# Kernel tuning notes

Hardware: AMD Instinct MI355X
Metric: run time of the kernel (lower is better)

Reference implementation:

```python
import jax, jax.numpy as jnp
import numpy as np

B, W, C, H = 2, 2048, 1024, 16
K = C // H  # 64
LN_EPS = 1e-5


def setup_inputs() -> dict:
    key = jax.random.key(0)
    ks = jax.random.split(key, 8)
    return {
        "seq1": jax.random.normal(ks[0], (B, W, C), jnp.float32),
        "seq2": jax.random.normal(ks[1], (B, W, C), jnp.float32),
        "ln_gamma": jnp.ones((C,), jnp.float32),
        "ln_beta": jnp.zeros((C,), jnp.float32),
        "q_proj": jax.random.normal(ks[2], (H, C, K), jnp.float32) * 0.02,
        "k_proj": jax.random.normal(ks[3], (H, C, K), jnp.float32) * 0.02,
        "v_proj": jax.random.normal(ks[4], (H, C, K), jnp.float32) * 0.02,
        "mixer_w": jax.random.normal(ks[5], (C, C), jnp.float32) * 0.02,
        "mixer_b": jnp.zeros((C,), jnp.float32),
    }


def _layernorm(x, gamma, beta):
    mu = jnp.mean(x, axis=-1, keepdims=True)
    var = jnp.mean(jnp.square(x - mu), axis=-1, keepdims=True)
    return (x - mu) * jax.lax.rsqrt(var + LN_EPS) * gamma + beta


def reference(seq1, seq2, ln_gamma, ln_beta, q_proj, k_proj, v_proj, mixer_w, mixer_b):
    x1 = _layernorm(seq1, ln_gamma, ln_beta)  # [B,W,C]
    x2 = _layernorm(seq2, ln_gamma, ln_beta)
    # per-head projections: [B,W,C] x [H,C,K] -> [B,H,W,K]
    q = jnp.einsum("bwc,hck->bhwk", x1, q_proj)
    k = jnp.einsum("bwc,hck->bhwk", x2, k_proj)
    v = jnp.einsum("bwc,hck->bhwk", x2, v_proj)
    scores = jnp.einsum("bhqk,bhmk->bhqm", q, k) / jnp.sqrt(jnp.float32(K))
    # causal mask (is_decoder=True)
    causal = jnp.tril(jnp.ones((W, W), bool))
    scores = jnp.where(causal[None, None], scores, jnp.float32(-jnp.inf))
    probs = jax.nn.softmax(scores, axis=-1)
    out = jnp.einsum("bhqm,bhmk->bhqk", probs, v)  # [B,H,W,K]
    out = out.transpose(0, 2, 1, 3).reshape(B, W, C)  # [B,W,C]
    return out @ mixer_w.T + mixer_b
```

## Files before the change

kernel.cpp:

```cpp
#include <hip/hip_runtime.h>
#include <math.h>

#define B_ 2
#define W_ 2048
#define C_ 1024
#define H_ 16
#define K_ 64
#define LN_EPS 1e-5f

typedef __attribute__((ext_vector_type(8))) short short8;
typedef __attribute__((ext_vector_type(4))) float float4v;

#if __has_builtin(__builtin_amdgcn_exp2f)
#define EXP2(x) __builtin_amdgcn_exp2f(x)
#else
#define EXP2(x) exp2f(x)
#endif

__device__ inline unsigned short f2bf(float f) {
  unsigned u = __float_as_uint(f);
  u += 0x7fffu + ((u >> 16) & 1u);
  return (unsigned short)(u >> 16);
}

__device__ inline float max3f(float a, float b, float c) {
  return fmaxf(fmaxf(a, b), c);
}

__device__ __forceinline__ void gload_lds16(const short* g, short* l) {
  __builtin_amdgcn_global_load_lds(
      (const __attribute__((address_space(1))) void*)g,
      (__attribute__((address_space(3))) void*)l, 16, 0, 0);
}

__device__ inline float2 block_sum2(float a, float b) {
  __shared__ float2 sb[4];
  #pragma unroll
  for (int o = 32; o > 0; o >>= 1) {
    a += __shfl_down(a, o, 64);
    b += __shfl_down(b, o, 64);
  }
  int lane = threadIdx.x & 63, wid = threadIdx.x >> 6;
  if (lane == 0) { sb[wid].x = a; sb[wid].y = b; }
  __syncthreads();
  float2 r;
  r.x = (sb[0].x + sb[1].x) + (sb[2].x + sb[3].x);
  r.y = (sb[0].y + sb[1].y) + (sb[2].y + sb[3].y);
  __syncthreads();
  return r;
}

__global__ __launch_bounds__(256) void ln_kernel(
    const float* __restrict__ seq1, const float* __restrict__ seq2,
    const float* __restrict__ gamma, const float* __restrict__ beta,
    short* __restrict__ x1b, short* __restrict__ x2b) {
  int row = blockIdx.x;
  const int nrows = B_ * W_;
  bool first = row < nrows;
  const float* src = first ? seq1 : seq2;
  short* dst = first ? x1b : x2b;
  int r = first ? row : row - nrows;

  const float4* p = (const float4*)(src + (size_t)r * C_);
  float4 v = p[threadIdx.x];
  float s1 = (v.x + v.y) + (v.z + v.w);
  float s2 = (v.x * v.x + v.y * v.y) + (v.z * v.z + v.w * v.w);
  float2 s = block_sum2(s1, s2);
  float mean = s.x * (1.0f / C_);
  float var = s.y * (1.0f / C_) - mean * mean;
  float rstd = rsqrtf(var + LN_EPS);

  float4 g = ((const float4*)gamma)[threadIdx.x];
  float4 b = ((const float4*)beta)[threadIdx.x];
  uint2 o;
  o.x = (unsigned)f2bf((v.x - mean) * rstd * g.x + b.x) |
        ((unsigned)f2bf((v.y - mean) * rstd * g.y + b.y) << 16);
  o.y = (unsigned)f2bf((v.z - mean) * rstd * g.z + b.z) |
        ((unsigned)f2bf((v.w - mean) * rstd * g.w + b.w) << 16);
  ((uint2*)(dst + (size_t)r * C_))[threadIdx.x] = o;
}

__global__ __launch_bounds__(256) void wprep_kernel(
    const float* __restrict__ qp, const float* __restrict__ kp,
    const float* __restrict__ vp, const float* __restrict__ wm,
    short* __restrict__ wqt, short* __restrict__ wkt, short* __restrict__ wvt,
    short* __restrict__ wmb) {
  int cb = blockIdx.x, h = blockIdx.y, which = blockIdx.z;
  int t = threadIdx.x;

  if (which == 3) {
    int blk = h * 16 + cb;
    #pragma unroll
    for (int j = 0; j < 4; ++j) {
      int gid = blk * 1024 + j * 256 + t;
      float4 v = ((const float4*)wm)[gid];
      uint2 o;
      o.x = (unsigned)f2bf(v.x) | ((unsigned)f2bf(v.y) << 16);
      o.y = (unsigned)f2bf(v.z) | ((unsigned)f2bf(v.w) << 16);
      ((uint2*)wmb)[gid] = o;
    }
    return;
  }

  const float* P = (which == 0 ? qp : (which == 1 ? kp : vp)) + (size_t)h * C_ * K_;
  short* Wt = (which == 0 ? wqt : (which == 1 ? wkt : wvt));
  float scale = (which == 0) ? 0.125f * 1.4426950408889634f : 1.0f;

  __shared__ float Ls[64][65];
  {
    int cr = t >> 2, ks = (t & 3) * 16;
    const float* src = P + (size_t)(cb * 64 + cr) * K_ + ks;
    #pragma unroll
    for (int j = 0; j < 4; ++j) {
      float4 v = *(const float4*)(src + j * 4);
      Ls[cr][ks + j * 4 + 0] = v.x; Ls[cr][ks + j * 4 + 1] = v.y;
      Ls[cr][ks + j * 4 + 2] = v.z; Ls[cr][ks + j * 4 + 3] = v.w;
    }
  }
  __syncthreads();
  int kr = t >> 2, cs = (t & 3) * 16;
  unsigned u[8];
  #pragma unroll
  for (int i = 0; i < 8; ++i) {
    float a = Ls[cs + 2 * i][kr] * scale;
    float b = Ls[cs + 2 * i + 1][kr] * scale;
    u[i] = (unsigned)f2bf(a) | ((unsigned)f2bf(b) << 16);
  }
  short* dst = Wt + ((size_t)h * 64 + kr) * C_ + cb * 64 + cs;
  uint4 p0; p0.x = u[0]; p0.y = u[1]; p0.z = u[2]; p0.w = u[3];
  uint4 p1; p1.x = u[4]; p1.y = u[5]; p1.z = u[6]; p1.w = u[7];
  *(uint4*)dst = p0;
  *(uint4*)(dst + 8) = p1;
}

__device__ __forceinline__ void gemm_core(
    const short* __restrict__ A, const short* __restrict__ Bt,
    int arow0, int brow0, short* As, short* Bs, float4v acc[4][4]) {
  int tid = threadIdx.x;
  int wave = tid >> 6, lane = tid & 63;
  int lr = lane >> 3, lc = lane & 7;
  int sc = lc ^ lr;
  int wr = wave >> 1, wc = wave & 1;
  int lg = lane >> 4, ll = lane & 15;

  #pragma unroll
  for (int mi = 0; mi < 4; ++mi)
    #pragma unroll
    for (int ni = 0; ni < 4; ++ni) {
      acc[mi][ni][0] = 0.f; acc[mi][ni][1] = 0.f;
      acc[mi][ni][2] = 0.f; acc[mi][ni][3] = 0.f;
    }

  for (int k0 = 0; k0 < C_; k0 += 64) {
    __syncthreads();
    #pragma unroll
    for (int j = 0; j < 4; ++j) {
      int seg = wave * 4 + j;
      int r = seg * 8 + lr;
      gload_lds16(A + (size_t)(arow0 + r) * C_ + k0 + sc * 8, As + seg * 512);
      gload_lds16(Bt + (size_t)(brow0 + r) * C_ + k0 + sc * 8, Bs + seg * 512);
    }
    __syncthreads();
    #pragma unroll
    for (int kc = 0; kc < 2; ++kc) {
      int cc = kc * 4 + lg;
      short8 af[4], bf[4];
      #pragma unroll
      for (int mi = 0; mi < 4; ++mi) {
        int m = wr * 64 + mi * 16 + ll;
        af[mi] = *(const short8*)&As[m * 64 + ((cc ^ (m & 7)) << 3)];
      }
      #pragma unroll
      for (int ni = 0; ni < 4; ++ni) {
        int n = wc * 64 + ni * 16 + ll;
        bf[ni] = *(const short8*)&Bs[n * 64 + ((cc ^ (n & 7)) << 3)];
      }
      #pragma unroll
      for (int mi = 0; mi < 4; ++mi)
        #pragma unroll
        for (int ni = 0; ni < 4; ++ni)
          acc[mi][ni] = __builtin_amdgcn_mfma_f32_16x16x32_bf16(
              af[mi], bf[ni], acc[mi][ni], 0, 0, 0);
    }
  }
}

__device__ __forceinline__ void gemm_core64(
    const short* __restrict__ A, const short* __restrict__ Bt,
    int arow0, int brow0, short* As, short* Bs, float4v acc[2][4]) {
  int tid = threadIdx.x;
  int wave = tid >> 6, lane = tid & 63;
  int lr = lane >> 3, lc = lane & 7;
  int sc = lc ^ lr;
  int wr = wave >> 1, wc = wave & 1;
  int lg = lane >> 4, ll = lane & 15;

  #pragma unroll
  for (int mi = 0; mi < 2; ++mi)
    #pragma unroll
    for (int ni = 0; ni < 4; ++ni) {
      acc[mi][ni][0] = 0.f; acc[mi][ni][1] = 0.f;
      acc[mi][ni][2] = 0.f; acc[mi][ni][3] = 0.f;
    }

  for (int k0 = 0; k0 < C_; k0 += 64) {
    __syncthreads();
    #pragma unroll
    for (int j = 0; j < 2; ++j) {
      int seg = wave * 2 + j;
      int r = seg * 8 + lr;
      gload_lds16(A + (size_t)(arow0 + r) * C_ + k0 + sc * 8, As + seg * 512);
    }
    #pragma unroll
    for (int j = 0; j < 4; ++j) {
      int seg = wave * 4 + j;
      int r = seg * 8 + lr;
      gload_lds16(Bt + (size_t)(brow0 + r) * C_ + k0 + sc * 8, Bs + seg * 512);
    }
    __syncthreads();
    #pragma unroll
    for (int kc = 0; kc < 2; ++kc) {
      int cc = kc * 4 + lg;
      short8 af[2], bf[4];
      #pragma unroll
      for (int mi = 0; mi < 2; ++mi) {
        int m = wr * 32 + mi * 16 + ll;
        af[mi] = *(const short8*)&As[m * 64 + ((cc ^ (m & 7)) << 3)];
      }
      #pragma unroll
      for (int ni = 0; ni < 4; ++ni) {
        int n = wc * 64 + ni * 16 + ll;
        bf[ni] = *(const short8*)&Bs[n * 64 + ((cc ^ (n & 7)) << 3)];
      }
      #pragma unroll
      for (int mi = 0; mi < 2; ++mi)
        #pragma unroll
        for (int ni = 0; ni < 4; ++ni)
          acc[mi][ni] = __builtin_amdgcn_mfma_f32_16x16x32_bf16(
              af[mi], bf[ni], acc[mi][ni], 0, 0, 0);
    }
  }
}

__global__ __launch_bounds__(256, 3) void gemm_qkv_kernel(
    const short* __restrict__ x1b, const short* __restrict__ x2b,
    const short* __restrict__ wqt, const short* __restrict__ wkt,
    const short* __restrict__ wvt,
    short* __restrict__ qb, short* __restrict__ kb, short* __restrict__ vtb) {
  __shared__ short smem[128 * 132];
  short* As = smem;
  short* Bs = smem + 8192;
  int z = blockIdx.z;
  const short *A, *Bt;
  int arow0, brow0;
  if (z == 0)      { A = x1b; Bt = wqt; arow0 = blockIdx.x * 128; brow0 = blockIdx.y * 128; }
  else if (z == 1) { A = x2b; Bt = wkt; arow0 = blockIdx.x * 128; brow0 = blockIdx.y * 128; }
  else             { A = wvt; Bt = x2b; arow0 = blockIdx.y * 128; brow0 = blockIdx.x * 128; }

  float4v acc[4][4];
  gemm_core(A, Bt, arow0, brow0, As, Bs, acc);

  int tid = threadIdx.x;
  int wave = tid >> 6, lane = tid & 63;
  int wr = wave >> 1, wc = wave & 1, lg = lane >> 4, ll = lane & 15;

  __syncthreads();
  #pragma unroll
  for (int mi = 0; mi < 4; ++mi)
    #pragma unroll
    for (int ni = 0; ni < 4; ++ni)
      #pragma unroll
      for (int r2 = 0; r2 < 4; ++r2)
        smem[(wr * 64 + mi * 16 + lg * 4 + r2) * 132 + wc * 64 + ni * 16 + ll] =
            (short)f2bf(acc[mi][ni][r2]);
  __syncthreads();

  if (z <= 1) {
    short* O = (z == 0) ? qb : kb;
    int hb = brow0 >> 6;
    #pragma unroll
    for (int p = 0; p < 8; ++p) {
      int r = p * 16 + (tid >> 4);
      int seg = tid & 15;
      int m = arow0 + r, b = m >> 11, w = m & (W_ - 1);
      int half = seg >> 3, kkseg = seg & 7;
      const short* src = &smem[r * 132 + seg * 8];
      uint2 lo = *(const uint2*)src;
      uint2 hi = *(const uint2*)(src + 4);
      uint4 val; val.x = lo.x; val.y = lo.y; val.z = hi.x; val.w = hi.y;
      *(uint4*)(O + ((size_t)(b * H_ + hb + half) * W_ + w) * K_ + kkseg * 8) = val;
    }
  } else {
    int b = brow0 >> 11, w0 = brow0 & (W_ - 1);
    #pragma unroll
    for (int p = 0; p < 8; ++p) {
      int r = p * 16 + (tid >> 4);
      int seg = tid & 15;
      int mg = arow0 + r, h = mg >> 6, kk = mg & 63;
      const short* src = &smem[r * 132 + seg * 8];
      uint2 lo = *(const uint2*)src;
      uint2 hi = *(const uint2*)(src + 4);
      uint4 val; val.x = lo.x; val.y = lo.y; val.z = hi.x; val.w = hi.y;
      *(uint4*)(vtb + ((size_t)(b * H_ + h) * K_ + kk) * W_ + w0 + seg * 8) = val;
    }
  }
}

__global__ __launch_bounds__(256, 3) void gemm_mix_kernel(
    const short* __restrict__ attnb, const short* __restrict__ wmb,
    const float* __restrict__ bias, float* __restrict__ out) {
  __shared__ short As[64 * 64], Bs[128 * 64];
  int arow0 = blockIdx.x * 64, brow0 = blockIdx.y * 128;
  float4v acc[2][4];
  gemm_core64(attnb, wmb, arow0, brow0, As, Bs, acc);

  int wave = threadIdx.x >> 6, lane = threadIdx.x & 63;
  int wr = wave >> 1, wc = wave & 1, lg = lane >> 4, ll = lane & 15;
  #pragma unroll
  for (int mi = 0; mi < 2; ++mi)
    #pragma unroll
    for (int ni = 0; ni < 4; ++ni) {
      int n = brow0 + wc * 64 + ni * 16 + ll;
      float bv = bias[n];
      #pragma unroll
      for (int r2 = 0; r2 < 4; ++r2) {
        int m = arow0 + wr * 32 + mi * 16 + lg * 4 + r2;
        out[(size_t)m * C_ + n] = acc[mi][ni][r2] + bv;
      }
    }
}

__global__ __launch_bounds__(256, 3) void attn_mfma_kernel(
    const short* __restrict__ q, const short* __restrict__ k,
    const short* __restrict__ vt, short* __restrict__ out) {
  int bh = blockIdx.x;
  int b = bh >> 4, h = bh & 15;
  int s = blockIdx.y;
  int qt = (s < 16) ? (31 - s) : (s - 16);
  int wave = threadIdx.x >> 6;
  int lane = threadIdx.x & 63;
  int lg = lane >> 4, ll = lane & 15;

  __shared__ short Ks[2][64 * 64];
  __shared__ short Vs[2][64 * 64];
  __shared__ short Ps[4][16 * 72];

  const short* qp = q + (size_t)bh * W_ * K_;
  const short* kp = k + (size_t)bh * W_ * K_;
  const short* vb = vt + (size_t)bh * K_ * W_;

  int qrow = qt * 64 + wave * 16 + ll;
  short8 aq[2];
  #pragma unroll
  for (int kc = 0; kc < 2; ++kc)
    aq[kc] = *(const short8*)(qp + (size_t)qrow * K_ + kc * 32 + lg * 8);

  short8 ones;
  #pragma unroll
  for (int i = 0; i < 8; ++i) ones[i] = (short)0x3F80;

  float4v o[4];
  #pragma unroll
  for (int ct = 0; ct < 4; ++ct) {
    o[ct][0] = 0.f; o[ct][1] = 0.f; o[ct][2] = 0.f; o[ct][3] = 0.f;
  }
  float4v lsum;
  lsum[0] = 0.f; lsum[1] = 0.f; lsum[2] = 0.f; lsum[3] = 0.f;
  float m = -INFINITY;

  int nkt = qt + 1;

  #define STAGE(kt, buf)                                                   \
    {                                                                      \
      const short* kbase = kp + (size_t)(kt) * 64 * K_;                    \
      const short* vbase = vb + (kt) * 64;                                 \
      _Pragma("unroll")                                                    \
      for (int j = 0; j < 2; ++j) {                                        \
        int sdx = j * 256 + (int)threadIdx.x;                              \
        int mm = sdx >> 3, c7 = sdx & 7;                                   \
        int gc = c7 ^ (mm & 7);                                            \
        gload_lds16(kbase + (size_t)mm * K_ + gc * 8, &Ks[buf][sdx * 8]);  \
        gload_lds16(vbase + (size_t)mm * W_ + gc * 8, &Vs[buf][sdx * 8]);  \
      }                                                                    \
    }

  STAGE(0, 0);
  for (int kt = 0; kt < nkt; ++kt) {
    int cur = kt & 1;
    asm volatile("s_waitcnt vmcnt(0) lgkmcnt(0)\ns_barrier" ::: "memory");
    if (kt + 1 < nkt) STAGE(kt + 1, cur ^ 1);

    float4v st[4];
    __builtin_amdgcn_s_setprio(1);
    #pragma unroll
    for (int nt = 0; nt < 4; ++nt) {
      st[nt][0] = 0.f; st[nt][1] = 0.f; st[nt][2] = 0.f; st[nt][3] = 0.f;
      int n = nt * 16 + ll;
      #pragma unroll
      for (int kc = 0; kc < 2; ++kc) {
        int cc = kc * 4 + lg;
        short8 bk = *(const short8*)&Ks[cur][n * 64 + ((cc ^ (n & 7)) << 3)];
        st[nt] = __builtin_amdgcn_mfma_f32_16x16x32_bf16(bk, aq[kc], st[nt], 0, 0, 0);
      }
    }
    __builtin_amdgcn_s_setprio(0);

    short8 bv[4][2];
    #pragma unroll
    for (int ct = 0; ct < 4; ++ct) {
      int c = ct * 16 + ll;
      #pragma unroll
      for (int kc = 0; kc < 2; ++kc) {
        int cc = kc * 4 + lg;
        bv[ct][kc] = *(const short8*)&Vs[cur][c * 64 + ((cc ^ (c & 7)) << 3)];
      }
    }

    if (kt == qt) {
      #pragma unroll
      for (int nt = 0; nt < 4; ++nt) {
        int keyb = nt * 16 + lg * 4;
        #pragma unroll
        for (int r = 0; r < 4; ++r)
          if (keyb + r > wave * 16 + ll) st[nt][r] = -INFINITY;
      }
    }

    float ma = max3f(st[0][0], st[0][1], st[0][2]);
    float mb = max3f(st[0][3], st[1][0], st[1][1]);
    float mc = max3f(st[1][2], st[1][3], st[2][0]);
    float md = max3f(st[2][1], st[2][2], st[2][3]);
    float me = max3f(st[3][0], st[3][1], st[3][2]);
    float lm = fmaxf(max3f(ma, mb, mc), max3f(md, me, st[3][3]));
    lm = fmaxf(lm, __shfl_xor(lm, 16, 64));
    lm = fmaxf(lm, __shfl_xor(lm, 32, 64));
    if (!__all(lm <= m + 8.f)) {
      float nm = fmaxf(m, lm);
      float al = EXP2(m - nm);
      m = nm;
      lsum[0] *= al; lsum[1] *= al; lsum[2] *= al; lsum[3] *= al;
      #pragma unroll
      for (int ct = 0; ct < 4; ++ct) {
        o[ct][0] *= al; o[ct][1] *= al; o[ct][2] *= al; o[ct][3] *= al;
      }
    }

    float p[4][4];
    #pragma unroll
    for (int nt = 0; nt < 4; ++nt)
      #pragma unroll
      for (int r = 0; r < 4; ++r)
        p[nt][r] = EXP2(st[nt][r] - m);

    short* myP = &Ps[wave][ll * 72];
    #pragma unroll
    for (int nt = 0; nt < 4; ++nt) {
      uint2 w;
      w.x = (unsigned)f2bf(p[nt][0]) | ((unsigned)f2bf(p[nt][1]) << 16);
      w.y = (unsigned)f2bf(p[nt][2]) | ((unsigned)f2bf(p[nt][3]) << 16);
      *(uint2*)(myP + nt * 16 + lg * 4) = w;
    }
    __builtin_amdgcn_s_waitcnt(0xC07F);
    short8 bp0 = *(const short8*)(myP + lg * 8);
    short8 bp1 = *(const short8*)(myP + 32 + lg * 8);

    __builtin_amdgcn_s_setprio(1);
    lsum = __builtin_amdgcn_mfma_f32_16x16x32_bf16(ones, bp0, lsum, 0, 0, 0);
    lsum = __builtin_amdgcn_mfma_f32_16x16x32_bf16(ones, bp1, lsum, 0, 0, 0);
    #pragma unroll
    for (int ct = 0; ct < 4; ++ct) {
      o[ct] = __builtin_amdgcn_mfma_f32_16x16x32_bf16(bv[ct][0], bp0, o[ct], 0, 0, 0);
      o[ct] = __builtin_amdgcn_mfma_f32_16x16x32_bf16(bv[ct][1], bp1, o[ct], 0, 0, 0);
    }
    __builtin_amdgcn_s_setprio(0);
  }
  #undef STAGE

  float invl = 1.0f / lsum[0];
  size_t orow = ((size_t)(b * W_ + qrow)) * C_ + h * K_;
  #pragma unroll
  for (int ct = 0; ct < 4; ++ct) {
    uint2 w;
    w.x = (unsigned)f2bf(o[ct][0] * invl) | ((unsigned)f2bf(o[ct][1] * invl) << 16);
    w.y = (unsigned)f2bf(o[ct][2] * invl) | ((unsigned)f2bf(o[ct][3] * invl) << 16);
    *(uint2*)(out + orow + ct * 16 + lg * 4) = w;
  }
}

extern "C" void kernel_launch(void* const* d_in, const int* in_sizes, int n_in,
                              void* d_out, int out_size, void* d_ws, size_t ws_size,
                              hipStream_t stream) {
  const float* seq1  = (const float*)d_in[0];
  const float* seq2  = (const float*)d_in[1];
  const float* gamma = (const float*)d_in[2];
  const float* beta  = (const float*)d_in[3];
  const float* qp    = (const float*)d_in[4];
  const float* kp    = (const float*)d_in[5];
  const float* vp    = (const float*)d_in[6];
  const float* wm    = (const float*)d_in[7];
  const float* mb    = (const float*)d_in[8];
  float* out = (float*)d_out;

  char* ws = (char*)d_ws;
  const size_t NROW = (size_t)B_ * W_;
  const size_t XB = NROW * C_ * sizeof(short);
  const size_t WB = (size_t)C_ * C_ * sizeof(short);
  short* x1b = (short*)(ws);
  short* x2b = (short*)(ws + XB);
  short* qb  = (short*)(ws + 2 * XB);
  short* kb  = (short*)(ws + 3 * XB);
  short* vtb = (short*)(ws + 4 * XB);
  short* wqt = (short*)(ws + 5 * XB);
  short* wkt = (short*)(ws + 5 * XB + WB);
  short* wvt = (short*)(ws + 5 * XB + 2 * WB);
  short* wmb = (short*)(ws + 5 * XB + 3 * WB);
  short* attnb = (short*)(ws + 5 * XB + 4 * WB);

  wprep_kernel<<<dim3(C_ / 64, H_, 4), dim3(256), 0, stream>>>(
      qp, kp, vp, wm, wqt, wkt, wvt, wmb);
  ln_kernel<<<dim3(2 * (unsigned)NROW), dim3(256), 0, stream>>>(
      seq1, seq2, gamma, beta, x1b, x2b);
  gemm_qkv_kernel<<<dim3(32, 8, 3), dim3(256), 0, stream>>>(
      x1b, x2b, wqt, wkt, wvt, qb, kb, vtb);
  attn_mfma_kernel<<<dim3(32, 32), dim3(256), 0, stream>>>(
      qb, kb, vtb, attnb);
  gemm_mix_kernel<<<dim3(64, 8), dim3(256), 0, stream>>>(attnb, wmb, mb, out);
}
```

Baseline: 193.0 us.

## Split attention work per wave into 32-query by 32-key quadrants with cross-wave merge

Each wave now handles 32 query rows against half of each 64-key tile instead of 16 query rows against the whole tile. Every K fragment loaded from LDS is reused for two query blocks, and each V fragment covers only half of the key dimension. This cuts LDS read traffic per MFMA and gives more independent MFMA chains. The price is a final cross-wave softmax merge through shared memory: max and sum exchange, rescaling, and summing partial outputs. That adds barriers, extra LDS use and more accumulator registers, which may hurt occupancy at 3 blocks per CU.

Measured after the change: 198.7 us. 3.0% more time.

```diff
diff --git a/kernel.cpp b/kernel.cpp
--- a/kernel.cpp
+++ b/kernel.cpp
@@ -338,50 +338,60 @@
   int s = blockIdx.y;
   int qt = (s < 16) ? (31 - s) : (s - 16);
   int wave = threadIdx.x >> 6;
+  int khalf = wave & 1, qhalf = wave >> 1;
   int lane = threadIdx.x & 63;
   int lg = lane >> 4, ll = lane & 15;
 
-  __shared__ short Ks[2][64 * 64];
-  __shared__ short Vs[2][64 * 64];
-  __shared__ short Ps[4][16 * 72];
+  __shared__ __align__(16) long long smemU[5376];
+  short* smem = (short*)smemU;
+  short* KsB = smem;
+  short* VsB = smem + 8192;
+  short* myP = smem + 16384 + wave * 1280;
+  __shared__ float mS[4][2][16], lS[4][2][16];
 
   const short* qp = q + (size_t)bh * W_ * K_;
   const short* kp = k + (size_t)bh * W_ * K_;
   const short* vb = vt + (size_t)bh * K_ * W_;
 
-  int qrow = qt * 64 + wave * 16 + ll;
-  short8 aq[2];
-  #pragma unroll
-  for (int kc = 0; kc < 2; ++kc)
-    aq[kc] = *(const short8*)(qp + (size_t)qrow * K_ + kc * 32 + lg * 8);
+  short8 aq[2][2];
+  #pragma unroll
+  for (int qb2 = 0; qb2 < 2; ++qb2)
+    #pragma unroll
+    for (int kc = 0; kc < 2; ++kc)
+      aq[qb2][kc] = *(const short8*)(
+          qp + (size_t)(qt * 64 + qhalf * 32 + qb2 * 16 + ll) * K_ + kc * 32 + lg * 8);
 
   short8 ones;
   #pragma unroll
   for (int i = 0; i < 8; ++i) ones[i] = (short)0x3F80;
 
-  float4v o[4];
-  #pragma unroll
-  for (int ct = 0; ct < 4; ++ct) {
-    o[ct][0] = 0.f; o[ct][1] = 0.f; o[ct][2] = 0.f; o[ct][3] = 0.f;
-  }
-  float4v lsum;
-  lsum[0] = 0.f; lsum[1] = 0.f; lsum[2] = 0.f; lsum[3] = 0.f;
-  float m = -INFINITY;
+  float4v o[4][2];
+  #pragma unroll
+  for (int ct = 0; ct < 4; ++ct)
+    #pragma unroll
+    for (int qb2 = 0; qb2 < 2; ++qb2) {
+      o[ct][qb2][0] = 0.f; o[ct][qb2][1] = 0.f;
+      o[ct][qb2][2] = 0.f; o[ct][qb2][3] = 0.f;
+    }
+  float4v lsum[2];
+  lsum[0][0] = 0.f; lsum[0][1] = 0.f; lsum[0][2] = 0.f; lsum[0][3] = 0.f;
+  lsum[1][0] = 0.f; lsum[1][1] = 0.f; lsum[1][2] = 0.f; lsum[1][3] = 0.f;
+  float m0 = -1e37f, m1 = -1e37f;
 
   int nkt = qt + 1;
 
-  #define STAGE(kt, buf)                                                   \
-    {                                                                      \
-      const short* kbase = kp + (size_t)(kt) * 64 * K_;                    \
-      const short* vbase = vb + (kt) * 64;                                 \
-      _Pragma("unroll")                                                    \
-      for (int j = 0; j < 2; ++j) {                                        \
-        int sdx = j * 256 + (int)threadIdx.x;                              \
-        int mm = sdx >> 3, c7 = sdx & 7;                                   \
-        int gc = c7 ^ (mm & 7);                                            \
-        gload_lds16(kbase + (size_t)mm * K_ + gc * 8, &Ks[buf][sdx * 8]);  \
-        gload_lds16(vbase + (size_t)mm * W_ + gc * 8, &Vs[buf][sdx * 8]);  \
-      }                                                                    \
+  #define STAGE(kt, buf)                                                     \
+    {                                                                        \
+      const short* kbase = kp + (size_t)(kt) * 64 * K_;                      \
+      const short* vbase = vb + (kt) * 64;                                   \
+      _Pragma("unroll")                                                      \
+      for (int j = 0; j < 2; ++j) {                                          \
+        int sdx = j * 256 + (int)threadIdx.x;                                \
+        int mm = sdx >> 3, c7 = sdx & 7;                                     \
+        int gc = c7 ^ (mm & 7);                                              \
+        gload_lds16(kbase + (size_t)mm * K_ + gc * 8, KsB + (buf) * 4096 + sdx * 8); \
+        gload_lds16(vbase + (size_t)mm * W_ + gc * 8, VsB + (buf) * 4096 + sdx * 8); \
+      }                                                                      \
     }
 
   STAGE(0, 0);
@@ -390,100 +400,150 @@
     asm volatile("s_waitcnt vmcnt(0) lgkmcnt(0)\ns_barrier" ::: "memory");
     if (kt + 1 < nkt) STAGE(kt + 1, cur ^ 1);
 
-    float4v st[4];
+    float4v st[2][2];
     __builtin_amdgcn_s_setprio(1);
     #pragma unroll
-    for (int nt = 0; nt < 4; ++nt) {
-      st[nt][0] = 0.f; st[nt][1] = 0.f; st[nt][2] = 0.f; st[nt][3] = 0.f;
-      int n = nt * 16 + ll;
+    for (int kb2 = 0; kb2 < 2; ++kb2) {
+      st[kb2][0][0] = 0.f; st[kb2][0][1] = 0.f; st[kb2][0][2] = 0.f; st[kb2][0][3] = 0.f;
+      st[kb2][1][0] = 0.f; st[kb2][1][1] = 0.f; st[kb2][1][2] = 0.f; st[kb2][1][3] = 0.f;
+      int n = khalf * 32 + kb2 * 16 + ll;
       #pragma unroll
       for (int kc = 0; kc < 2; ++kc) {
         int cc = kc * 4 + lg;
-        short8 bk = *(const short8*)&Ks[cur][n * 64 + ((cc ^ (n & 7)) << 3)];
-        st[nt] = __builtin_amdgcn_mfma_f32_16x16x32_bf16(bk, aq[kc], st[nt], 0, 0, 0);
+        short8 ak = *(const short8*)&KsB[cur * 4096 + n * 64 + ((cc ^ (n & 7)) << 3)];
+        st[kb2][0] = __builtin_amdgcn_mfma_f32_16x16x32_bf16(ak, aq[0][kc], st[kb2][0], 0, 0, 0);
+        st[kb2][1] = __builtin_amdgcn_mfma_f32_16x16x32_bf16(ak, aq[1][kc], st[kb2][1], 0, 0, 0);
       }
     }
     __builtin_amdgcn_s_setprio(0);
 
-    short8 bv[4][2];
+    short8 bv[4];
     #pragma unroll
     for (int ct = 0; ct < 4; ++ct) {
       int c = ct * 16 + ll;
-      #pragma unroll
-      for (int kc = 0; kc < 2; ++kc) {
-        int cc = kc * 4 + lg;
-        bv[ct][kc] = *(const short8*)&Vs[cur][c * 64 + ((cc ^ (c & 7)) << 3)];
-      }
+      int cc = khalf * 4 + lg;
+      bv[ct] = *(const short8*)&VsB[cur * 4096 + c * 64 + ((cc ^ (c & 7)) << 3)];
     }
 
     if (kt == qt) {
       #pragma unroll
-      for (int nt = 0; nt < 4; ++nt) {
-        int keyb = nt * 16 + lg * 4;
+      for (int kb2 = 0; kb2 < 2; ++kb2) {
+        int keyb = khalf * 32 + kb2 * 16 + lg * 4;
         #pragma unroll
-        for (int r = 0; r < 4; ++r)
-          if (keyb + r > wave * 16 + ll) st[nt][r] = -INFINITY;
-      }
-    }
-
-    float ma = max3f(st[0][0], st[0][1], st[0][2]);
-    float mb = max3f(st[0][3], st[1][0], st[1][1]);
-    float mc = max3f(st[1][2], st[1][3], st[2][0]);
-    float md = max3f(st[2][1], st[2][2], st[2][3]);
-    float me = max3f(st[3][0], st[3][1], st[3][2]);
-    float lm = fmaxf(max3f(ma, mb, mc), max3f(md, me, st[3][3]));
-    lm = fmaxf(lm, __shfl_xor(lm, 16, 64));
-    lm = fmaxf(lm, __shfl_xor(lm, 32, 64));
-    if (!__all(lm <= m + 8.f)) {
-      float nm = fmaxf(m, lm);
-      float al = EXP2(m - nm);
-      m = nm;
-      lsum[0] *= al; lsum[1] *= al; lsum[2] *= al; lsum[3] *= al;
+        for (int r = 0; r < 4; ++r) {
+          int key = keyb + r;
+          if (key > qhalf * 32 + ll) st[kb2][0][r] = -INFINITY;
+          if (key > qhalf * 32 + 16 + ll) st[kb2][1][r] = -INFINITY;
+        }
+      }
+    }
+
+    float lm0 = fmaxf(max3f(st[0][0][0], st[0][0][1], st[0][0][2]),
+                      fmaxf(max3f(st[0][0][3], st[1][0][0], st[1][0][1]),
+                            max3f(st[1][0][2], st[1][0][3], -INFINITY)));
+    float lm1 = fmaxf(max3f(st[0][1][0], st[0][1][1], st[0][1][2]),
+                      fmaxf(max3f(st[0][1][3], st[1][1][0], st[1][1][1]),
+                            max3f(st[1][1][2], st[1][1][3], -INFINITY)));
+    lm0 = fmaxf(lm0, __shfl_xor(lm0, 16, 64));
+    lm0 = fmaxf(lm0, __shfl_xor(lm0, 32, 64));
+    lm1 = fmaxf(lm1, __shfl_xor(lm1, 16, 64));
+    lm1 = fmaxf(lm1, __shfl_xor(lm1, 32, 64));
+    if (!__all((lm0 <= m0 + 8.f) && (lm1 <= m1 + 8.f))) {
+      float nm0 = fmaxf(m0, lm0), nm1 = fmaxf(m1, lm1);
+      float al0 = EXP2(m0 - nm0), al1 = EXP2(m1 - nm1);
+      m0 = nm0; m1 = nm1;
+      lsum[0][0] *= al0; lsum[0][1] *= al0; lsum[0][2] *= al0; lsum[0][3] *= al0;
+      lsum[1][0] *= al1; lsum[1][1] *= al1; lsum[1][2] *= al1; lsum[1][3] *= al1;
       #pragma unroll
       for (int ct = 0; ct < 4; ++ct) {
-        o[ct][0] *= al; o[ct][1] *= al; o[ct][2] *= al; o[ct][3] *= al;
-      }
-    }
-
-    float p[4][4];
-    #pragma unroll
-    for (int nt = 0; nt < 4; ++nt)
-      #pragma unroll
-      for (int r = 0; r < 4; ++r)
-        p[nt][r] = EXP2(st[nt][r] - m);
-
-    short* myP = &Ps[wave][ll * 72];
-    #pragma unroll
-    for (int nt = 0; nt < 4; ++nt) {
+        o[ct][0][0] *= al0; o[ct][0][1] *= al0; o[ct][0][2] *= al0; o[ct][0][3] *= al0;
+        o[ct][1][0] *= al1; o[ct][1][1] *= al1; o[ct][1][2] *= al1; o[ct][1][3] *= al1;
+      }
+    }
+
+    #pragma unroll
+    for (int kb2 = 0; kb2 < 2; ++kb2) {
+      {
+        float e0 = EXP2(st[kb2][0][0] - m0), e1 = EXP2(st[kb2][0][1] - m0);
+        float e2 = EXP2(st[kb2][0][2] - m0), e3 = EXP2(st[kb2][0][3] - m0);
+        uint2 w;
+        w.x = (unsigned)f2bf(e0) | ((unsigned)f2bf(e1) << 16);
+        w.y = (unsigned)f2bf(e2) | ((unsigned)f2bf(e3) << 16);
+        *(uint2*)(myP + ll * 40 + kb2 * 16 + lg * 4) = w;
+      }
+      {
+        float e0 = EXP2(st[kb2][1][0] - m1), e1 = EXP2(st[kb2][1][1] - m1);
+        float e2 = EXP2(st[kb2][1][2] - m1), e3 = EXP2(st[kb2][1][3] - m1);
+        uint2 w;
+        w.x = (unsigned)f2bf(e0) | ((unsigned)f2bf(e1) << 16);
+        w.y = (unsigned)f2bf(e2) | ((unsigned)f2bf(e3) << 16);
+        *(uint2*)(myP + (16 + ll) * 40 + kb2 * 16 + lg * 4) = w;
+      }
+    }
+    __builtin_amdgcn_s_waitcnt(0xC07F);
+    short8 bp0 = *(const short8*)(myP + ll * 40 + lg * 8);
+    short8 bp1 = *(const short8*)(myP + (16 + ll) * 40 + lg * 8);
+
+    __builtin_amdgcn_s_setprio(1);
+    lsum[0] = __builtin_amdgcn_mfma_f32_16x16x32_bf16(ones, bp0, lsum[0], 0, 0, 0);
+    lsum[1] = __builtin_amdgcn_mfma_f32_16x16x32_bf16(ones, bp1, lsum[1], 0, 0, 0);
+    #pragma unroll
+    for (int ct = 0; ct < 4; ++ct) {
+      o[ct][0] = __builtin_amdgcn_mfma_f32_16x16x32_bf16(bv[ct], bp0, o[ct][0], 0, 0, 0);
+      o[ct][1] = __builtin_amdgcn_mfma_f32_16x16x32_bf16(bv[ct], bp1, o[ct][1], 0, 0, 0);
+    }
+    __builtin_amdgcn_s_setprio(0);
+  }
+  #undef STAGE
+
+  __syncthreads();
+  if (lg == 0) {
+    mS[wave][0][ll] = m0; mS[wave][1][ll] = m1;
+    lS[wave][0][ll] = lsum[0][0]; lS[wave][1][ll] = lsum[1][0];
+  }
+  __syncthreads();
+  int pw = wave ^ 1;
+  float pm0 = mS[pw][0][ll], pm1 = mS[pw][1][ll];
+  float pl0 = lS[pw][0][ll], pl1 = lS[pw][1][ll];
+  float ms0 = fmaxf(m0, pm0), ms1 = fmaxf(m1, pm1);
+  float sc0 = EXP2(m0 - ms0), sc1 = EXP2(m1 - ms1);
+  float lf0 = lsum[0][0] * sc0 + pl0 * EXP2(pm0 - ms0);
+  float lf1 = lsum[1][0] * sc1 + pl1 * EXP2(pm1 - ms1);
+
+  float* mb = (float*)smemU;
+  float* myb = mb + (size_t)(wave * 2176);
+  #pragma unroll
+  for (int ct = 0; ct < 4; ++ct)
+    #pragma unroll
+    for (int qb2 = 0; qb2 < 2; ++qb2) {
+      float sc = qb2 ? sc1 : sc0;
+      float4v v;
+      v[0] = o[ct][qb2][0] * sc; v[1] = o[ct][qb2][1] * sc;
+      v[2] = o[ct][qb2][2] * sc; v[3] = o[ct][qb2][3] * sc;
+      *(float4v*)&myb[(qb2 * 16 + ll) * 68 + ct * 16 + lg * 4] = v;
+    }
+  __syncthreads();
+
+  float* b0 = mb + (size_t)((qhalf * 2 + 0) * 2176);
+  float* b1 = mb + (size_t)((qhalf * 2 + 1) * 2176);
+  #pragma unroll
+  for (int qb2 = 0; qb2 < 2; ++qb2) {
+    float invl = 1.0f / (qb2 ? lf1 : lf0);
+    int qrow = qt * 64 + qhalf * 32 + qb2 * 16 + ll;
+    size_t orow = ((size_t)(b * W_ + qrow)) * C_ + h * K_;
+    #pragma unroll
+    for (int ct2 = 0; ct2 < 2; ++ct2) {
+      int chan = khalf * 32 + ct2 * 16 + lg * 4;
+      int idx = (qb2 * 16 + ll) * 68 + chan;
+      float4v vA = *(const float4v*)&b0[idx];
+      float4v vB = *(const float4v*)&b1[idx];
       uint2 w;
-      w.x = (unsigned)f2bf(p[nt][0]) | ((unsigned)f2bf(p[nt][1]) << 16);
-      w.y = (unsigned)f2bf(p[nt][2]) | ((unsigned)f2bf(p[nt][3]) << 16);
-      *(uint2*)(myP + nt * 16 + lg * 4) = w;
-    }
-    __builtin_amdgcn_s_waitcnt(0xC07F);
-    short8 bp0 = *(const short8*)(myP + lg * 8);
-    short8 bp1 = *(const short8*)(myP + 32 + lg * 8);
-
-    __builtin_amdgcn_s_setprio(1);
-    lsum = __builtin_amdgcn_mfma_f32_16x16x32_bf16(ones, bp0, lsum, 0, 0, 0);
-    lsum = __builtin_amdgcn_mfma_f32_16x16x32_bf16(ones, bp1, lsum, 0, 0, 0);
-    #pragma unroll
-    for (int ct = 0; ct < 4; ++ct) {
-      o[ct] = __builtin_amdgcn_mfma_f32_16x16x32_bf16(bv[ct][0], bp0, o[ct], 0, 0, 0);
-      o[ct] = __builtin_amdgcn_mfma_f32_16x16x32_bf16(bv[ct][1], bp1, o[ct], 0, 0, 0);
-    }
-    __builtin_amdgcn_s_setprio(0);
-  }
-  #undef STAGE
-
-  float invl = 1.0f / lsum[0];
-  size_t orow = ((size_t)(b * W_ + qrow)) * C_ + h * K_;
-  #pragma unroll
-  for (int ct = 0; ct < 4; ++ct) {
-    uint2 w;
-    w.x = (unsigned)f2bf(o[ct][0] * invl) | ((unsigned)f2bf(o[ct][1] * invl) << 16);
-    w.y = (unsigned)f2bf(o[ct][2] * invl) | ((unsigned)f2bf(o[ct][3] * invl) << 16);
-    *(uint2*)(out + orow + ct * 16 + lg * 4) = w;
+      w.x = (unsigned)f2bf((vA[0] + vB[0]) * invl) |
+            ((unsigned)f2bf((vA[1] + vB[1]) * invl) << 16);
+      w.y = (unsigned)f2bf((vA[2] + vB[2]) * invl) |
+            ((unsigned)f2bf((vA[3] + vB[3]) * invl) << 16);
+      *(uint2*)(out + orow + chan) = w;
+    }
   }
 }
 
```
